# Kernel tuning notes

Measured on AMD Instinct MI355X. Metric: run time of the kernel, lower is better.

Reference implementation:

```python
import jax, jax.numpy as jnp
import numpy as np
from jax.scipy.special import logsumexp

D = 256; H = 8; A = D // H
B_CONST = 0.9; P_MAX = 50000.0; P_MIN = 1e-4; TANH_RATE = 0.005; EPS = 1e-10
SCALE = 1.0 / np.sqrt(D)


def setup_inputs() -> dict:
    key = jax.random.key(0)
    ks = jax.random.split(key, 5)
    B, S = 2, 512
    context = jax.random.normal(ks[0], (B, S, D), dtype=jnp.float32)
    W_Q = jax.random.normal(ks[1], (D, D), dtype=jnp.float32) * (1.0 / np.sqrt(D))
    W_KV = jax.random.normal(ks[2], (2 * D, D), dtype=jnp.float32) * (1.0 / np.sqrt(D))
    W_out = jax.random.normal(ks[3], (D, D), dtype=jnp.float32) * (1.0 / np.sqrt(D))
    p_param = jax.random.normal(ks[4], (D,), dtype=jnp.float32) * 0.02
    return {"context": context, "W_Q": W_Q, "W_KV": W_KV, "W_out": W_out, "p_param": p_param}


def reference(context, W_Q, W_KV, W_out, p_param):
    B, S, _ = context.shape
    # projections (nn.Linear: x @ W.T)
    q = context @ W_Q.T                          # [B,S,D]
    kv = context @ W_KV.T                        # [B,S,2D]
    k, v = kv[..., :D], kv[..., D:]
    # scaled p: p_max*tanh(tanh_rate*p)+1, then replace exact zeros with p_min
    p = P_MAX * jnp.tanh(TANH_RATE * p_param) + 1.0
    p = p + (p == 0).astype(p.dtype) * P_MIN
    # minmax-normalize v over the key/sequence axis into [b, 1]
    v_max = jnp.max(v, axis=-2, keepdims=True)   # [B,1,D]
    v_min = jnp.min(v, axis=-2, keepdims=True)
    v = (1.0 - B_CONST) * (v - v_min) / (v_max - v_min + EPS) + B_CONST
    z = p * jnp.log(v)                           # [B,S,D]
    # split heads
    qh = q.reshape(B, S, H, A).transpose(0, 2, 1, 3)          # [B,H,S,A]
    kh = k.reshape(B, S, H, A).transpose(0, 2, 1, 3)          # [B,H,S,A]
    zh = z.reshape(B, S, H, A).transpose(0, 2, 1, 3)[:, :, None]  # [B,H,1,K,A]
    dot = jnp.einsum('bhqa,bhka->bhqk', qh, kh)
    w = jax.nn.log_softmax(dot * SCALE, axis=-1)              # [B,H,Q,K]
    # log-domain power mean: logsumexp over keys of log-weights + p*log(v)
    mean = logsumexp(w[..., None] + zh, axis=-2)              # [B,H,Q,A]
    mean = mean.transpose(0, 2, 1, 3).reshape(B, S, D)
    e = jnp.exp(mean / p)
    # invert v minmax normalization
    e = (e - B_CONST) * (v_max - v_min + EPS) / (1.0 - B_CONST) + v_min
    return e @ W_out.T
```

## Files before the change

### kernel.cpp

```cpp
#include <hip/hip_runtime.h>
#include <math.h>

#define DD 256
#define HH 8
#define AA 32
#define SS 512
#define BB 2
constexpr float BCONST      = 0.9f;
constexpr float ONE_MINUS_B = 0.1f;
constexpr float EPSF        = 1e-10f;
constexpr float SCALEF      = 0.0625f;
constexpr float FLTMAX      = 3.402823466e38f;

#define OFF_QKV    0
#define OFF_VP     786432
#define OFF_EW     1048576
#define OFF_PMIN   1310720
#define OFF_PMAX   1318912
#define OFF_VMIN   1327104
#define OFF_VRANGE 1327616
#define OFF_P      1328128

#define KB4(buf, row, col4) \
  (&(buf)[((row) << 5) | ((((col4) >> 2) ^ (((row) >> 2) & 7)) << 2)])

template<int TM, int TN, int RM, int RN, bool MM>
__global__ __launch_bounds__(256) void gemm_t(
    const float* __restrict__ A, const float* __restrict__ B0,
    const float* __restrict__ B1, int nsplit,
    float* __restrict__ C, int ldc, int K, int lda,
    float* __restrict__ pminP, float* __restrict__ pmaxP) {
  constexpr int LDT = 36;
  constexpr int CG  = TN / RN;
  constexpr int NA  = TM * 32 / 1024;
  constexpr int NB  = TN * 32 / 1024;
  __shared__ float As[TM][LDT];
  __shared__ float Bs[TN][LDT];
  const int i0 = blockIdx.x * TM;
  const int j0 = blockIdx.y * TN;
  const float* Bsrc = (j0 < nsplit) ? (B0 + (size_t)j0 * K)
                                    : (B1 + (size_t)(j0 - nsplit) * K);
  const int t  = threadIdx.x;
  const int lr = t >> 3;
  const int lc = (t & 7) << 2;
  const int tx = t % CG, ty = t / CG;

  float4 pa[NA], pb[NB];
#pragma unroll
  for (int u = 0; u < NA; ++u)
    pa[u] = *(const float4*)(A + (size_t)(i0 + lr + 32 * u) * lda + lc);
#pragma unroll
  for (int u = 0; u < NB; ++u)
    pb[u] = *(const float4*)(Bsrc + (size_t)(lr + 32 * u) * K + lc);

  float acc[RM][RN] = {};
  for (int k0 = 0; k0 < K; k0 += 32) {
    __syncthreads();
#pragma unroll
    for (int u = 0; u < NA; ++u) *(float4*)&As[lr + 32 * u][lc] = pa[u];
#pragma unroll
    for (int u = 0; u < NB; ++u) *(float4*)&Bs[lr + 32 * u][lc] = pb[u];
    __syncthreads();
    if (k0 + 32 < K) {
#pragma unroll
      for (int u = 0; u < NA; ++u)
        pa[u] = *(const float4*)(A + (size_t)(i0 + lr + 32 * u) * lda + k0 + 32 + lc);
#pragma unroll
      for (int u = 0; u < NB; ++u)
        pb[u] = *(const float4*)(Bsrc + (size_t)(lr + 32 * u) * K + k0 + 32 + lc);
    }
#pragma unroll
    for (int kk = 0; kk < 32; kk += 4) {
      float4 af[RM], bf[RN];
#pragma unroll
      for (int r = 0; r < RM; ++r) af[r] = *(const float4*)&As[ty * RM + r][kk];
#pragma unroll
      for (int c = 0; c < RN; ++c) bf[c] = *(const float4*)&Bs[tx + CG * c][kk];
#pragma unroll
      for (int r = 0; r < RM; ++r)
#pragma unroll
        for (int c = 0; c < RN; ++c)
          acc[r][c] += af[r].x * bf[c].x + af[r].y * bf[c].y +
                       af[r].z * bf[c].z + af[r].w * bf[c].w;
    }
  }
#pragma unroll
  for (int r = 0; r < RM; ++r)
#pragma unroll
    for (int c = 0; c < RN; ++c)
      C[(size_t)(i0 + ty * RM + r) * ldc + j0 + tx + CG * c] = acc[r][c];

  if (MM && j0 >= 512) {
    __syncthreads();
    float* mnb = &As[0][0];
    float* mxb = &Bs[0][0];
#pragma unroll
    for (int c = 0; c < RN; ++c) {
      float mn = acc[0][c], mx = acc[0][c];
#pragma unroll
      for (int r = 1; r < RM; ++r) {
        mn = fminf(mn, acc[r][c]);
        mx = fmaxf(mx, acc[r][c]);
      }
      mnb[(tx + CG * c) * 17 + ty] = mn;
      mxb[(tx + CG * c) * 17 + ty] = mx;
    }
    __syncthreads();
    if (t < TN) {
      float mn = mnb[t * 17], mx = mxb[t * 17];
#pragma unroll
      for (int i = 1; i < 16; ++i) {
        mn = fminf(mn, mnb[t * 17 + i]);
        mx = fmaxf(mx, mxb[t * 17 + i]);
      }
      const int bx = i0 >> 5;
      pminP[bx * 256 + (j0 - 512) + t] = mn;
      pmaxP[bx * 256 + (j0 - 512) + t] = mx;
    }
  }
}

__global__ __launch_bounds__(256) void vpk(
    const float* __restrict__ qkv, const float* __restrict__ pminP,
    const float* __restrict__ pmaxP, const float* __restrict__ p_param,
    float* __restrict__ vp, float* __restrict__ vminw,
    float* __restrict__ vrangew, float* __restrict__ pw) {
  const int blk = blockIdx.x;
  const int b = blk >> 9, s = blk & 511;
  const int d = threadIdx.x;
  float mn = pminP[(b * 16) * 256 + d];
  float mx = pmaxP[(b * 16) * 256 + d];
#pragma unroll
  for (int c = 1; c < 16; ++c) {
    mn = fminf(mn, pminP[(b * 16 + c) * 256 + d]);
    mx = fmaxf(mx, pmaxP[(b * 16 + c) * 256 + d]);
  }
  float p = 50000.0f * tanhf(0.005f * p_param[d]) + 1.0f;
  if (p == 0.0f) p = 0.0001f;
  const float range = mx - mn + EPSF;
  const float v  = qkv[((size_t)(b * 512 + s)) * 768 + 512 + d];
  const float vn = (ONE_MINUS_B * (v - mn)) / range + BCONST;
  vp[(size_t)blk * 256 + d] = expm1f(p * logf(vn));
  if (s == 0) { vminw[b * 256 + d] = mn; vrangew[b * 256 + d] = range; }
  if (blk == 0) pw[d] = p;
}

__global__ __launch_bounds__(256) void attn_k(
    const float* __restrict__ qkv, const float* __restrict__ vp,
    const float* __restrict__ pw, const float* __restrict__ vminw,
    const float* __restrict__ vrangew, float* __restrict__ ew) {
  __shared__ float qs[32][36];
  __shared__ float sc[32 * 516];
  __shared__ float kb[512 * 32];
  __shared__ float red[32];
  const int bh  = blockIdx.y;
  const int b   = bh >> 3, h = bh & 7;
  const int q0g = blockIdx.x * 32;
  const int t   = threadIdx.x;
  const int srow = t >> 3, scol4 = (t & 7) << 2;

  {
    const int q = t >> 3, c4 = (t & 7) << 2;
    float4 qv = *(const float4*)(qkv + ((size_t)(b * 512 + q0g + q)) * 768 + h * 32 + c4);
    qv.x *= SCALEF; qv.y *= SCALEF; qv.z *= SCALEF; qv.w *= SCALEF;
    *(float4*)&qs[q][c4] = qv;
  }
#pragma unroll 8
  for (int u = 0; u < 16; ++u) {
    const int r = srow + 32 * u;
    float4 v = *(const float4*)(qkv + ((size_t)(b * 512 + r)) * 768 + 256 + h * 32 + scol4);
    *(float4*)KB4(kb, r, scol4) = v;
  }
  __syncthreads();

  {
    const int qgw = t >> 6;
    const int kg  = t & 63;
    float s8[8][8] = {};
#pragma unroll 2
    for (int kk = 0; kk < 32; kk += 4) {
      float4 qf[8], kf1[4], kf2[4];
#pragma unroll
      for (int r = 0; r < 8; ++r) qf[r] = *(const float4*)&qs[qgw + 4 * r][kk];
#pragma unroll
      for (int c = 0; c < 4; ++c) {
        kf1[c] = *(const float4*)KB4(kb, kg * 4 + c, kk);
        kf2[c] = *(const float4*)KB4(kb, 256 + kg * 4 + c, kk);
      }
#pragma unroll
      for (int r = 0; r < 8; ++r)
#pragma unroll
        for (int c = 0; c < 4; ++c) {
          s8[r][c]     += qf[r].x * kf1[c].x + qf[r].y * kf1[c].y +
                          qf[r].z * kf1[c].z + qf[r].w * kf1[c].w;
          s8[r][4 + c] += qf[r].x * kf2[c].x + qf[r].y * kf2[c].y +
                          qf[r].z * kf2[c].z + qf[r].w * kf2[c].w;
        }
    }
    float rs[8];
#pragma unroll
    for (int r = 0; r < 8; ++r) {
      float s = 0.f;
#pragma unroll
      for (int c = 0; c < 8; ++c) {
        s8[r][c] = __expf(s8[r][c]);
        s += s8[r][c];
      }
      rs[r] = s;
    }
#pragma unroll
    for (int m = 1; m < 64; m <<= 1)
#pragma unroll
      for (int r = 0; r < 8; ++r) rs[r] += __shfl_xor(rs[r], m);
    if ((t & 63) == 0)
#pragma unroll
      for (int r = 0; r < 8; ++r) red[qgw + 4 * r] = rs[r];
#pragma unroll
    for (int r = 0; r < 8; ++r) {
      const int rq = qgw + 4 * r;
      *(float4*)&sc[rq * 516 + kg * 4] =
          make_float4(s8[r][0], s8[r][1], s8[r][2], s8[r][3]);
      *(float4*)&sc[rq * 516 + 256 + kg * 4] =
          make_float4(s8[r][4], s8[r][5], s8[r][6], s8[r][7]);
    }
  }
  __syncthreads();

#pragma unroll 8
  for (int u = 0; u < 16; ++u) {
    const int r = srow + 32 * u;
    float4 v = *(const float4*)(vp + ((size_t)(b * 512 + r)) * 256 + h * 32 + scol4);
    *(float4*)KB4(kb, r, scol4) = v;
  }
  __syncthreads();

  const int ag  = t & 7;
  const int qg3 = (t >> 3) & 3;
  const int ks  = t >> 5;
  float a3[8][4] = {};
#pragma unroll 2
  for (int g = 0; g < 16; ++g) {
    const int kbase = ks * 64 + g * 4;
    float4 sq[8], vf[4];
#pragma unroll
    for (int r = 0; r < 8; ++r)
      sq[r] = *(const float4*)&sc[(qg3 + 4 * r) * 516 + kbase];
#pragma unroll
    for (int c = 0; c < 4; ++c)
      vf[c] = *(const float4*)KB4(kb, kbase + c, ag * 4);
#pragma unroll
    for (int r = 0; r < 8; ++r) {
      a3[r][0] += sq[r].x * vf[0].x + sq[r].y * vf[1].x + sq[r].z * vf[2].x + sq[r].w * vf[3].x;
      a3[r][1] += sq[r].x * vf[0].y + sq[r].y * vf[1].y + sq[r].z * vf[2].y + sq[r].w * vf[3].y;
      a3[r][2] += sq[r].x * vf[0].z + sq[r].y * vf[1].z + sq[r].z * vf[2].z + sq[r].w * vf[3].z;
      a3[r][3] += sq[r].x * vf[0].w + sq[r].y * vf[1].w + sq[r].z * vf[2].w + sq[r].w * vf[3].w;
    }
  }

#pragma unroll
  for (int r = 0; r < 8; ++r)
#pragma unroll
    for (int c = 0; c < 4; ++c)
      a3[r][c] += __shfl_xor(a3[r][c], 32);
  __syncthreads();
  float* part = &kb[0];
  if ((t & 32) == 0) {
    const int w = t >> 6;
#pragma unroll
    for (int r = 0; r < 8; ++r)
#pragma unroll
      for (int c = 0; c < 4; ++c)
        part[w * 1152 + (qg3 + 4 * r) * 36 + ag * 4 + c] = a3[r][c];
  }
  __syncthreads();

  {
    const int q = t >> 3, a0 = (t & 7) << 2;
    const int d0 = h * 32 + a0;
    const float invT = 1.0f / red[q];
    float4 s0 = *(const float4*)&part[q * 36 + a0];
    float4 s1 = *(const float4*)&part[1152 + q * 36 + a0];
    float4 s2 = *(const float4*)&part[2304 + q * 36 + a0];
    float4 s3 = *(const float4*)&part[3456 + q * 36 + a0];
    const float4 pp = *(const float4*)(pw + d0);
    const float4 vr = *(const float4*)(vrangew + b * 256 + d0);
    const float4 vm = *(const float4*)(vminw + b * 256 + d0);
    float4 o;
    o.x = (expf(log1pf((s0.x + s1.x + s2.x + s3.x) * invT) / pp.x) - BCONST) * vr.x / ONE_MINUS_B + vm.x;
    o.y = (expf(log1pf((s0.y + s1.y + s2.y + s3.y) * invT) / pp.y) - BCONST) * vr.y / ONE_MINUS_B + vm.y;
    o.z = (expf(log1pf((s0.z + s1.z + s2.z + s3.z) * invT) / pp.z) - BCONST) * vr.z / ONE_MINUS_B + vm.z;
    o.w = (expf(log1pf((s0.w + s1.w + s2.w + s3.w) * invT) / pp.w) - BCONST) * vr.w / ONE_MINUS_B + vm.w;
    *(float4*)(ew + ((size_t)(b * 512 + q0g + q)) * 256 + d0) = o;
  }
}

extern "C" void kernel_launch(void* const* d_in, const int* in_sizes, int n_in,
                              void* d_out, int out_size, void* d_ws, size_t ws_size,
                              hipStream_t stream) {
  const float* ctx  = (const float*)d_in[0];
  const float* WQ   = (const float*)d_in[1];
  const float* WKV  = (const float*)d_in[2];
  const float* WOUT = (const float*)d_in[3];
  const float* PP   = (const float*)d_in[4];
  float* ws      = (float*)d_ws;
  float* qkv     = ws + OFF_QKV;
  float* vp      = ws + OFF_VP;
  float* ew      = ws + OFF_EW;
  float* pminP   = ws + OFF_PMIN;
  float* pmaxP   = ws + OFF_PMAX;
  float* vminw   = ws + OFF_VMIN;
  float* vrangew = ws + OFF_VRANGE;
  float* pw      = ws + OFF_P;
  float* out     = (float*)d_out;

  gemm_t<32, 64, 2, 4, true><<<dim3(32, 12), 256, 0, stream>>>(
      ctx, WQ, WKV, 256, qkv, 768, 256, 256, pminP, pmaxP);
  vpk<<<1024, 256, 0, stream>>>(qkv, pminP, pmaxP, PP, vp, vminw, vrangew, pw);
  attn_k<<<dim3(16, 16), 256, 0, stream>>>(qkv, vp, pw, vminw, vrangew, ew);
  gemm_t<32, 32, 2, 2, false><<<dim3(32, 8), 256, 0, stream>>>(
      ew, WOUT, WOUT, 1 << 30, out, 256, 256, 256, nullptr, nullptr);
}
```

Measured before the change: 107.3 us.

## Fuse all four stages into one persistent kernel with software grid barriers

Replaces the four separate launches (QKV GEMM, v-power transform, attention, output GEMM) with one 256-block persistent kernel that separates the stages with atomic-counter grid barriers. The QKV GEMM is retiled to 32x96 tiles and the v-transform is redistributed so each stage maps onto exactly 256 blocks. The aim is to remove launch gaps and inter-kernel drain between the small stages. In exchange it relies on all 256 blocks being co-resident, adds spin-wait barrier cost with system-scope fences, and resets the barrier with a magic-flag handshake that could race across repeated calls.

Measured after the change: 204.2 us. +90.3%, slower.

```diff
diff --git a/kernel.cpp b/kernel.cpp
--- a/kernel.cpp
+++ b/kernel.cpp
@@ -1,296 +1,368 @@
 #include <hip/hip_runtime.h>
 #include <math.h>
 
-#define DD 256
-#define HH 8
-#define AA 32
-#define SS 512
-#define BB 2
 constexpr float BCONST      = 0.9f;
 constexpr float ONE_MINUS_B = 0.1f;
 constexpr float EPSF        = 1e-10f;
 constexpr float SCALEF      = 0.0625f;
-constexpr float FLTMAX      = 3.402823466e38f;
-
-#define OFF_QKV    0
-#define OFF_VP     786432
-#define OFF_EW     1048576
-#define OFF_PMIN   1310720
-#define OFF_PMAX   1318912
-#define OFF_VMIN   1327104
-#define OFF_VRANGE 1327616
-#define OFF_P      1328128
+
+#define OFF_QKV   0
+#define OFF_VP    786432
+#define OFF_EW    1048576
+#define OFF_PMIN  1310720
+#define OFF_PMAX  1318912
+#define OFF_VMIN  1327104
+#define OFF_VRG   1327616
+#define OFF_P     1328128
+#define OFF_BAR   8388608
+
+#define BAR_MAGIC 0x9E3779B9u
 
 #define KB4(buf, row, col4) \
   (&(buf)[((row) << 5) | ((((col4) >> 2) ^ (((row) >> 2) & 7)) << 2)])
 
-template<int TM, int TN, int RM, int RN, bool MM>
-__global__ __launch_bounds__(256) void gemm_t(
-    const float* __restrict__ A, const float* __restrict__ B0,
-    const float* __restrict__ B1, int nsplit,
-    float* __restrict__ C, int ldc, int K, int lda,
-    float* __restrict__ pminP, float* __restrict__ pmaxP) {
-  constexpr int LDT = 36;
-  constexpr int CG  = TN / RN;
-  constexpr int NA  = TM * 32 / 1024;
-  constexpr int NB  = TN * 32 / 1024;
-  __shared__ float As[TM][LDT];
-  __shared__ float Bs[TN][LDT];
-  const int i0 = blockIdx.x * TM;
-  const int j0 = blockIdx.y * TN;
-  const float* Bsrc = (j0 < nsplit) ? (B0 + (size_t)j0 * K)
-                                    : (B1 + (size_t)(j0 - nsplit) * K);
-  const int t  = threadIdx.x;
-  const int lr = t >> 3;
-  const int lc = (t & 7) << 2;
-  const int tx = t % CG, ty = t / CG;
-
-  float4 pa[NA], pb[NB];
-#pragma unroll
-  for (int u = 0; u < NA; ++u)
-    pa[u] = *(const float4*)(A + (size_t)(i0 + lr + 32 * u) * lda + lc);
-#pragma unroll
-  for (int u = 0; u < NB; ++u)
-    pb[u] = *(const float4*)(Bsrc + (size_t)(lr + 32 * u) * K + lc);
-
-  float acc[RM][RN] = {};
-  for (int k0 = 0; k0 < K; k0 += 32) {
-    __syncthreads();
-#pragma unroll
-    for (int u = 0; u < NA; ++u) *(float4*)&As[lr + 32 * u][lc] = pa[u];
-#pragma unroll
-    for (int u = 0; u < NB; ++u) *(float4*)&Bs[lr + 32 * u][lc] = pb[u];
-    __syncthreads();
-    if (k0 + 32 < K) {
-#pragma unroll
-      for (int u = 0; u < NA; ++u)
-        pa[u] = *(const float4*)(A + (size_t)(i0 + lr + 32 * u) * lda + k0 + 32 + lc);
-#pragma unroll
-      for (int u = 0; u < NB; ++u)
-        pb[u] = *(const float4*)(Bsrc + (size_t)(lr + 32 * u) * K + k0 + 32 + lc);
-    }
-#pragma unroll
-    for (int kk = 0; kk < 32; kk += 4) {
-      float4 af[RM], bf[RN];
-#pragma unroll
-      for (int r = 0; r < RM; ++r) af[r] = *(const float4*)&As[ty * RM + r][kk];
-#pragma unroll
-      for (int c = 0; c < RN; ++c) bf[c] = *(const float4*)&Bs[tx + CG * c][kk];
-#pragma unroll
-      for (int r = 0; r < RM; ++r)
-#pragma unroll
-        for (int c = 0; c < RN; ++c)
-          acc[r][c] += af[r].x * bf[c].x + af[r].y * bf[c].y +
-                       af[r].z * bf[c].z + af[r].w * bf[c].w;
-    }
-  }
-#pragma unroll
-  for (int r = 0; r < RM; ++r)
-#pragma unroll
-    for (int c = 0; c < RN; ++c)
-      C[(size_t)(i0 + ty * RM + r) * ldc + j0 + tx + CG * c] = acc[r][c];
-
-  if (MM && j0 >= 512) {
-    __syncthreads();
-    float* mnb = &As[0][0];
-    float* mxb = &Bs[0][0];
-#pragma unroll
-    for (int c = 0; c < RN; ++c) {
-      float mn = acc[0][c], mx = acc[0][c];
-#pragma unroll
-      for (int r = 1; r < RM; ++r) {
-        mn = fminf(mn, acc[r][c]);
-        mx = fmaxf(mx, acc[r][c]);
-      }
-      mnb[(tx + CG * c) * 17 + ty] = mn;
-      mxb[(tx + CG * c) * 17 + ty] = mx;
-    }
-    __syncthreads();
-    if (t < TN) {
-      float mn = mnb[t * 17], mx = mxb[t * 17];
-#pragma unroll
-      for (int i = 1; i < 16; ++i) {
-        mn = fminf(mn, mnb[t * 17 + i]);
-        mx = fmaxf(mx, mxb[t * 17 + i]);
-      }
-      const int bx = i0 >> 5;
-      pminP[bx * 256 + (j0 - 512) + t] = mn;
-      pmaxP[bx * 256 + (j0 - 512) + t] = mx;
-    }
-  }
+__device__ __forceinline__ void gridbar(unsigned* cnt, unsigned* flag,
+                                        unsigned gen, bool first) {
+  __syncthreads();
+  if (threadIdx.x == 0) {
+    __threadfence_system();
+    if (first) {
+      while (__hip_atomic_load(flag, __ATOMIC_ACQUIRE,
+                               __HIP_MEMORY_SCOPE_SYSTEM) != BAR_MAGIC) {
+        __builtin_amdgcn_s_sleep(2);
+      }
+    }
+    __hip_atomic_fetch_add(cnt, 1u, __ATOMIC_ACQ_REL,
+                           __HIP_MEMORY_SCOPE_SYSTEM);
+    const unsigned tgt = 256u * gen;
+    while (__hip_atomic_load(cnt, __ATOMIC_ACQUIRE,
+                             __HIP_MEMORY_SCOPE_SYSTEM) < tgt) {
+      __builtin_amdgcn_s_sleep(2);
+    }
+    __threadfence_system();
+  }
+  __syncthreads();
 }
 
-__global__ __launch_bounds__(256) void vpk(
-    const float* __restrict__ qkv, const float* __restrict__ pminP,
-    const float* __restrict__ pmaxP, const float* __restrict__ p_param,
-    float* __restrict__ vp, float* __restrict__ vminw,
-    float* __restrict__ vrangew, float* __restrict__ pw) {
+__global__ __launch_bounds__(256) void fused_k(
+    const float* __restrict__ ctx, const float* __restrict__ WQ,
+    const float* __restrict__ WKV, const float* __restrict__ WOUT,
+    const float* __restrict__ PP, float* __restrict__ ws,
+    float* __restrict__ out) {
+  __shared__ float S[34080];
   const int blk = blockIdx.x;
-  const int b = blk >> 9, s = blk & 511;
-  const int d = threadIdx.x;
-  float mn = pminP[(b * 16) * 256 + d];
-  float mx = pmaxP[(b * 16) * 256 + d];
-#pragma unroll
-  for (int c = 1; c < 16; ++c) {
-    mn = fminf(mn, pminP[(b * 16 + c) * 256 + d]);
-    mx = fmaxf(mx, pmaxP[(b * 16 + c) * 256 + d]);
-  }
-  float p = 50000.0f * tanhf(0.005f * p_param[d]) + 1.0f;
-  if (p == 0.0f) p = 0.0001f;
-  const float range = mx - mn + EPSF;
-  const float v  = qkv[((size_t)(b * 512 + s)) * 768 + 512 + d];
-  const float vn = (ONE_MINUS_B * (v - mn)) / range + BCONST;
-  vp[(size_t)blk * 256 + d] = expm1f(p * logf(vn));
-  if (s == 0) { vminw[b * 256 + d] = mn; vrangew[b * 256 + d] = range; }
-  if (blk == 0) pw[d] = p;
-}
-
-__global__ __launch_bounds__(256) void attn_k(
-    const float* __restrict__ qkv, const float* __restrict__ vp,
-    const float* __restrict__ pw, const float* __restrict__ vminw,
-    const float* __restrict__ vrangew, float* __restrict__ ew) {
-  __shared__ float qs[32][36];
-  __shared__ float sc[32 * 516];
-  __shared__ float kb[512 * 32];
-  __shared__ float red[32];
-  const int bh  = blockIdx.y;
-  const int b   = bh >> 3, h = bh & 7;
-  const int q0g = blockIdx.x * 32;
   const int t   = threadIdx.x;
-  const int srow = t >> 3, scol4 = (t & 7) << 2;
+
+  float* qkv   = ws + OFF_QKV;
+  float* vp    = ws + OFF_VP;
+  float* ew    = ws + OFF_EW;
+  float* pminP = ws + OFF_PMIN;
+  float* pmaxP = ws + OFF_PMAX;
+  float* vminw = ws + OFF_VMIN;
+  float* vrgw  = ws + OFF_VRG;
+  float* pw    = ws + OFF_P;
+  unsigned* bar = (unsigned*)(ws + OFF_BAR);
+
+  if (blk == 0 && t == 0) {
+    __hip_atomic_store(&bar[0], 0u, __ATOMIC_RELAXED, __HIP_MEMORY_SCOPE_SYSTEM);
+    __threadfence_system();
+    __hip_atomic_store(&bar[1], BAR_MAGIC, __ATOMIC_RELEASE, __HIP_MEMORY_SCOPE_SYSTEM);
+  }
 
   {
-    const int q = t >> 3, c4 = (t & 7) << 2;
-    float4 qv = *(const float4*)(qkv + ((size_t)(b * 512 + q0g + q)) * 768 + h * 32 + c4);
-    qv.x *= SCALEF; qv.y *= SCALEF; qv.z *= SCALEF; qv.w *= SCALEF;
-    *(float4*)&qs[q][c4] = qv;
-  }
+    float (*As)[36] = (float (*)[36])S;
+    float (*Bs)[36] = (float (*)[36])(S + 1152);
+    const int rt = blk & 31, ct = blk >> 5;
+    const int i0 = rt * 32, j0 = ct * 96;
+    const int lr = t >> 3, lc = (t & 7) << 2;
+    const int tx = t & 15, ty = t >> 4;
+    const float* arow = ctx + (size_t)(i0 + lr) * 256;
+    const float* brow[3];
+#pragma unroll
+    for (int u = 0; u < 3; ++u) {
+      const int j = j0 + lr + 32 * u;
+      brow[u] = (j < 256) ? (WQ + (size_t)j * 256)
+                          : (WKV + (size_t)(j - 256) * 256);
+    }
+    float4 pa = *(const float4*)(arow + lc);
+    float4 pb[3];
+#pragma unroll
+    for (int u = 0; u < 3; ++u) pb[u] = *(const float4*)(brow[u] + lc);
+
+    float acc[2][6] = {};
+    for (int k0 = 0; k0 < 256; k0 += 32) {
+      __syncthreads();
+      *(float4*)&As[lr][lc] = pa;
+#pragma unroll
+      for (int u = 0; u < 3; ++u) *(float4*)&Bs[lr + 32 * u][lc] = pb[u];
+      __syncthreads();
+      if (k0 + 32 < 256) {
+        pa = *(const float4*)(arow + k0 + 32 + lc);
+#pragma unroll
+        for (int u = 0; u < 3; ++u)
+          pb[u] = *(const float4*)(brow[u] + k0 + 32 + lc);
+      }
+#pragma unroll
+      for (int kk = 0; kk < 32; kk += 4) {
+        float4 af[2], bf[6];
+#pragma unroll
+        for (int r = 0; r < 2; ++r) af[r] = *(const float4*)&As[ty * 2 + r][kk];
+#pragma unroll
+        for (int c = 0; c < 6; ++c) bf[c] = *(const float4*)&Bs[tx + 16 * c][kk];
+#pragma unroll
+        for (int r = 0; r < 2; ++r)
+#pragma unroll
+          for (int c = 0; c < 6; ++c)
+            acc[r][c] += af[r].x * bf[c].x + af[r].y * bf[c].y +
+                         af[r].z * bf[c].z + af[r].w * bf[c].w;
+      }
+    }
+#pragma unroll
+    for (int r = 0; r < 2; ++r)
+#pragma unroll
+      for (int c = 0; c < 6; ++c)
+        qkv[(size_t)(i0 + ty * 2 + r) * 768 + j0 + tx + 16 * c] = acc[r][c];
+
+    if (ct >= 5) {
+      __syncthreads();
+      float* mnb = S;
+      float* mxb = S + 1632;
+#pragma unroll
+      for (int c = 0; c < 6; ++c) {
+        mnb[(tx + 16 * c) * 17 + ty] = fminf(acc[0][c], acc[1][c]);
+        mxb[(tx + 16 * c) * 17 + ty] = fmaxf(acc[0][c], acc[1][c]);
+      }
+      __syncthreads();
+      if (t < 96) {
+        const int j = j0 + t;
+        if (j >= 512) {
+          float mn = mnb[t * 17], mx = mxb[t * 17];
+#pragma unroll
+          for (int i = 1; i < 16; ++i) {
+            mn = fminf(mn, mnb[t * 17 + i]);
+            mx = fmaxf(mx, mxb[t * 17 + i]);
+          }
+          pminP[rt * 256 + (j - 512)] = mn;
+          pmaxP[rt * 256 + (j - 512)] = mx;
+        }
+      }
+    }
+  }
+  gridbar(&bar[0], &bar[1], 1u, true);
+
+  {
+    float p = 50000.0f * tanhf(0.005f * PP[t]) + 1.0f;
+    if (p == 0.0f) p = 0.0001f;
+    if (blk == 0) pw[t] = p;
+#pragma unroll
+    for (int b = 0; b < 2; ++b) {
+      float mn = pminP[(b * 16) * 256 + t];
+      float mx = pmaxP[(b * 16) * 256 + t];
+#pragma unroll
+      for (int c = 1; c < 16; ++c) {
+        mn = fminf(mn, pminP[(b * 16 + c) * 256 + t]);
+        mx = fmaxf(mx, pmaxP[(b * 16 + c) * 256 + t]);
+      }
+      const float range = mx - mn + EPSF;
+      if (blk == 0) { vminw[b * 256 + t] = mn; vrgw[b * 256 + t] = range; }
+#pragma unroll
+      for (int i = 0; i < 2; ++i) {
+        const int s = blk + 256 * i;
+        const float v  = qkv[((size_t)(b * 512 + s)) * 768 + 512 + t];
+        const float vn = (ONE_MINUS_B * (v - mn)) / range + BCONST;
+        vp[((size_t)(b * 512 + s)) * 256 + t] = expm1f(p * logf(vn));
+      }
+    }
+  }
+  gridbar(&bar[0], &bar[1], 2u, false);
+
+  {
+    float* qs  = S;
+    float* sc  = S + 1152;
+    float* kb  = S + 17664;
+    float* red = S + 34048;
+    const int bh  = blk >> 4;
+    const int b   = bh >> 3, h = bh & 7;
+    const int q0g = (blk & 15) * 32;
+    const int srow = t >> 3, scol4 = (t & 7) << 2;
+
+    {
+      const int q = t >> 3, c4 = (t & 7) << 2;
+      float4 qv = *(const float4*)(qkv + ((size_t)(b * 512 + q0g + q)) * 768 + h * 32 + c4);
+      qv.x *= SCALEF; qv.y *= SCALEF; qv.z *= SCALEF; qv.w *= SCALEF;
+      *(float4*)&qs[q * 36 + c4] = qv;
+    }
 #pragma unroll 8
-  for (int u = 0; u < 16; ++u) {
-    const int r = srow + 32 * u;
-    float4 v = *(const float4*)(qkv + ((size_t)(b * 512 + r)) * 768 + 256 + h * 32 + scol4);
-    *(float4*)KB4(kb, r, scol4) = v;
-  }
-  __syncthreads();
+    for (int u = 0; u < 16; ++u) {
+      const int r = srow + 32 * u;
+      float4 v = *(const float4*)(qkv + ((size_t)(b * 512 + r)) * 768 + 256 + h * 32 + scol4);
+      *(float4*)KB4(kb, r, scol4) = v;
+    }
+    __syncthreads();
+
+    {
+      const int qgw = t >> 6;
+      const int kg  = t & 63;
+      float s8[8][8] = {};
+#pragma unroll 2
+      for (int kk = 0; kk < 32; kk += 4) {
+        float4 qf[8], kf1[4], kf2[4];
+#pragma unroll
+        for (int r = 0; r < 8; ++r) qf[r] = *(const float4*)&qs[(qgw + 4 * r) * 36 + kk];
+#pragma unroll
+        for (int c = 0; c < 4; ++c) {
+          kf1[c] = *(const float4*)KB4(kb, kg * 4 + c, kk);
+          kf2[c] = *(const float4*)KB4(kb, 256 + kg * 4 + c, kk);
+        }
+#pragma unroll
+        for (int r = 0; r < 8; ++r)
+#pragma unroll
+          for (int c = 0; c < 4; ++c) {
+            s8[r][c]     += qf[r].x * kf1[c].x + qf[r].y * kf1[c].y +
+                            qf[r].z * kf1[c].z + qf[r].w * kf1[c].w;
+            s8[r][4 + c] += qf[r].x * kf2[c].x + qf[r].y * kf2[c].y +
+                            qf[r].z * kf2[c].z + qf[r].w * kf2[c].w;
+          }
+      }
+      float rs[8];
+#pragma unroll
+      for (int r = 0; r < 8; ++r) {
+        float s = 0.f;
+#pragma unroll
+        for (int c = 0; c < 8; ++c) {
+          s8[r][c] = __expf(s8[r][c]);
+          s += s8[r][c];
+        }
+        rs[r] = s;
+      }
+#pragma unroll
+      for (int m = 1; m < 64; m <<= 1)
+#pragma unroll
+        for (int r = 0; r < 8; ++r) rs[r] += __shfl_xor(rs[r], m);
+      if ((t & 63) == 0)
+#pragma unroll
+        for (int r = 0; r < 8; ++r) red[qgw + 4 * r] = rs[r];
+#pragma unroll
+      for (int r = 0; r < 8; ++r) {
+        const int rq = qgw + 4 * r;
+        *(float4*)&sc[rq * 516 + kg * 4] =
+            make_float4(s8[r][0], s8[r][1], s8[r][2], s8[r][3]);
+        *(float4*)&sc[rq * 516 + 256 + kg * 4] =
+            make_float4(s8[r][4], s8[r][5], s8[r][6], s8[r][7]);
+      }
+    }
+    __syncthreads();
+
+#pragma unroll 8
+    for (int u = 0; u < 16; ++u) {
+      const int r = srow + 32 * u;
+      float4 v = *(const float4*)(vp + ((size_t)(b * 512 + r)) * 256 + h * 32 + scol4);
+      *(float4*)KB4(kb, r, scol4) = v;
+    }
+    __syncthreads();
+
+    const int ag  = t & 7;
+    const int qg3 = (t >> 3) & 3;
+    const int ks  = t >> 5;
+    float a3[8][4] = {};
+#pragma unroll 2
+    for (int g = 0; g < 16; ++g) {
+      const int kbase = ks * 64 + g * 4;
+      float4 sq[8], vf[4];
+#pragma unroll
+      for (int r = 0; r < 8; ++r)
+        sq[r] = *(const float4*)&sc[(qg3 + 4 * r) * 516 + kbase];
+#pragma unroll
+      for (int c = 0; c < 4; ++c)
+        vf[c] = *(const float4*)KB4(kb, kbase + c, ag * 4);
+#pragma unroll
+      for (int r = 0; r < 8; ++r) {
+        a3[r][0] += sq[r].x * vf[0].x + sq[r].y * vf[1].x + sq[r].z * vf[2].x + sq[r].w * vf[3].x;
+        a3[r][1] += sq[r].x * vf[0].y + sq[r].y * vf[1].y + sq[r].z * vf[2].y + sq[r].w * vf[3].y;
+        a3[r][2] += sq[r].x * vf[0].z + sq[r].y * vf[1].z + sq[r].z * vf[2].z + sq[r].w * vf[3].z;
+        a3[r][3] += sq[r].x * vf[0].w + sq[r].y * vf[1].w + sq[r].z * vf[2].w + sq[r].w * vf[3].w;
+      }
+    }
+#pragma unroll
+    for (int r = 0; r < 8; ++r)
+#pragma unroll
+      for (int c = 0; c < 4; ++c)
+        a3[r][c] += __shfl_xor(a3[r][c], 32);
+    __syncthreads();
+    float* part = kb;
+    if ((t & 32) == 0) {
+      const int w = t >> 6;
+#pragma unroll
+      for (int r = 0; r < 8; ++r)
+#pragma unroll
+        for (int c = 0; c < 4; ++c)
+          part[w * 1152 + (qg3 + 4 * r) * 36 + ag * 4 + c] = a3[r][c];
+    }
+    __syncthreads();
+
+    {
+      const int q = t >> 3, a0 = (t & 7) << 2;
+      const int d0 = h * 32 + a0;
+      const float invT = 1.0f / red[q];
+      float4 s0 = *(const float4*)&part[q * 36 + a0];
+      float4 s1 = *(const float4*)&part[1152 + q * 36 + a0];
+      float4 s2 = *(const float4*)&part[2304 + q * 36 + a0];
+      float4 s3 = *(const float4*)&part[3456 + q * 36 + a0];
+      const float4 pp = *(const float4*)(pw + d0);
+      const float4 vr = *(const float4*)(vrgw + b * 256 + d0);
+      const float4 vm = *(const float4*)(vminw + b * 256 + d0);
+      float4 o;
+      o.x = (expf(log1pf((s0.x + s1.x + s2.x + s3.x) * invT) / pp.x) - BCONST) * vr.x / ONE_MINUS_B + vm.x;
+      o.y = (expf(log1pf((s0.y + s1.y + s2.y + s3.y) * invT) / pp.y) - BCONST) * vr.y / ONE_MINUS_B + vm.y;
+      o.z = (expf(log1pf((s0.z + s1.z + s2.z + s3.z) * invT) / pp.z) - BCONST) * vr.z / ONE_MINUS_B + vm.z;
+      o.w = (expf(log1pf((s0.w + s1.w + s2.w + s3.w) * invT) / pp.w) - BCONST) * vr.w / ONE_MINUS_B + vm.w;
+      *(float4*)(ew + ((size_t)(b * 512 + q0g + q)) * 256 + d0) = o;
+    }
+  }
+  gridbar(&bar[0], &bar[1], 3u, false);
 
   {
-    const int qgw = t >> 6;
-    const int kg  = t & 63;
-    float s8[8][8] = {};
-#pragma unroll 2
-    for (int kk = 0; kk < 32; kk += 4) {
-      float4 qf[8], kf1[4], kf2[4];
-#pragma unroll
-      for (int r = 0; r < 8; ++r) qf[r] = *(const float4*)&qs[qgw + 4 * r][kk];
-#pragma unroll
-      for (int c = 0; c < 4; ++c) {
-        kf1[c] = *(const float4*)KB4(kb, kg * 4 + c, kk);
-        kf2[c] = *(const float4*)KB4(kb, 256 + kg * 4 + c, kk);
-      }
-#pragma unroll
-      for (int r = 0; r < 8; ++r)
-#pragma unroll
-        for (int c = 0; c < 4; ++c) {
-          s8[r][c]     += qf[r].x * kf1[c].x + qf[r].y * kf1[c].y +
-                          qf[r].z * kf1[c].z + qf[r].w * kf1[c].w;
-          s8[r][4 + c] += qf[r].x * kf2[c].x + qf[r].y * kf2[c].y +
-                          qf[r].z * kf2[c].z + qf[r].w * kf2[c].w;
-        }
-    }
-    float rs[8];
-#pragma unroll
-    for (int r = 0; r < 8; ++r) {
-      float s = 0.f;
-#pragma unroll
-      for (int c = 0; c < 8; ++c) {
-        s8[r][c] = __expf(s8[r][c]);
-        s += s8[r][c];
-      }
-      rs[r] = s;
-    }
-#pragma unroll
-    for (int m = 1; m < 64; m <<= 1)
-#pragma unroll
-      for (int r = 0; r < 8; ++r) rs[r] += __shfl_xor(rs[r], m);
-    if ((t & 63) == 0)
-#pragma unroll
-      for (int r = 0; r < 8; ++r) red[qgw + 4 * r] = rs[r];
-#pragma unroll
-    for (int r = 0; r < 8; ++r) {
-      const int rq = qgw + 4 * r;
-      *(float4*)&sc[rq * 516 + kg * 4] =
-          make_float4(s8[r][0], s8[r][1], s8[r][2], s8[r][3]);
-      *(float4*)&sc[rq * 516 + 256 + kg * 4] =
-          make_float4(s8[r][4], s8[r][5], s8[r][6], s8[r][7]);
-    }
-  }
-  __syncthreads();
-
-#pragma unroll 8
-  for (int u = 0; u < 16; ++u) {
-    const int r = srow + 32 * u;
-    float4 v = *(const float4*)(vp + ((size_t)(b * 512 + r)) * 256 + h * 32 + scol4);
-    *(float4*)KB4(kb, r, scol4) = v;
-  }
-  __syncthreads();
-
-  const int ag  = t & 7;
-  const int qg3 = (t >> 3) & 3;
-  const int ks  = t >> 5;
-  float a3[8][4] = {};
-#pragma unroll 2
-  for (int g = 0; g < 16; ++g) {
-    const int kbase = ks * 64 + g * 4;
-    float4 sq[8], vf[4];
-#pragma unroll
-    for (int r = 0; r < 8; ++r)
-      sq[r] = *(const float4*)&sc[(qg3 + 4 * r) * 516 + kbase];
-#pragma unroll
-    for (int c = 0; c < 4; ++c)
-      vf[c] = *(const float4*)KB4(kb, kbase + c, ag * 4);
-#pragma unroll
-    for (int r = 0; r < 8; ++r) {
-      a3[r][0] += sq[r].x * vf[0].x + sq[r].y * vf[1].x + sq[r].z * vf[2].x + sq[r].w * vf[3].x;
-      a3[r][1] += sq[r].x * vf[0].y + sq[r].y * vf[1].y + sq[r].z * vf[2].y + sq[r].w * vf[3].y;
-      a3[r][2] += sq[r].x * vf[0].z + sq[r].y * vf[1].z + sq[r].z * vf[2].z + sq[r].w * vf[3].z;
-      a3[r][3] += sq[r].x * vf[0].w + sq[r].y * vf[1].w + sq[r].z * vf[2].w + sq[r].w * vf[3].w;
-    }
-  }
-
-#pragma unroll
-  for (int r = 0; r < 8; ++r)
-#pragma unroll
-    for (int c = 0; c < 4; ++c)
-      a3[r][c] += __shfl_xor(a3[r][c], 32);
-  __syncthreads();
-  float* part = &kb[0];
-  if ((t & 32) == 0) {
-    const int w = t >> 6;
-#pragma unroll
-    for (int r = 0; r < 8; ++r)
-#pragma unroll
-      for (int c = 0; c < 4; ++c)
-        part[w * 1152 + (qg3 + 4 * r) * 36 + ag * 4 + c] = a3[r][c];
-  }
-  __syncthreads();
-
-  {
-    const int q = t >> 3, a0 = (t & 7) << 2;
-    const int d0 = h * 32 + a0;
-    const float invT = 1.0f / red[q];
-    float4 s0 = *(const float4*)&part[q * 36 + a0];
-    float4 s1 = *(const float4*)&part[1152 + q * 36 + a0];
-    float4 s2 = *(const float4*)&part[2304 + q * 36 + a0];
-    float4 s3 = *(const float4*)&part[3456 + q * 36 + a0];
-    const float4 pp = *(const float4*)(pw + d0);
-    const float4 vr = *(const float4*)(vrangew + b * 256 + d0);
-    const float4 vm = *(const float4*)(vminw + b * 256 + d0);
-    float4 o;
-    o.x = (expf(log1pf((s0.x + s1.x + s2.x + s3.x) * invT) / pp.x) - BCONST) * vr.x / ONE_MINUS_B + vm.x;
-    o.y = (expf(log1pf((s0.y + s1.y + s2.y + s3.y) * invT) / pp.y) - BCONST) * vr.y / ONE_MINUS_B + vm.y;
-    o.z = (expf(log1pf((s0.z + s1.z + s2.z + s3.z) * invT) / pp.z) - BCONST) * vr.z / ONE_MINUS_B + vm.z;
-    o.w = (expf(log1pf((s0.w + s1.w + s2.w + s3.w) * invT) / pp.w) - BCONST) * vr.w / ONE_MINUS_B + vm.w;
-    *(float4*)(ew + ((size_t)(b * 512 + q0g + q)) * 256 + d0) = o;
+    float (*As)[36] = (float (*)[36])S;
+    float (*Bs)[36] = (float (*)[36])(S + 1152);
+    const int rt = blk & 31, ct = blk >> 5;
+    const int i0 = rt * 32, j0 = ct * 32;
+    const int lr = t >> 3, lc = (t & 7) << 2;
+    const int tx = t & 15, ty = t >> 4;
+    const float* arow = ew + (size_t)(i0 + lr) * 256;
+    const float* brow = WOUT + (size_t)(j0 + lr) * 256;
+    float4 pa = *(const float4*)(arow + lc);
+    float4 pb = *(const float4*)(brow + lc);
+
+    float acc[2][2] = {};
+    for (int k0 = 0; k0 < 256; k0 += 32) {
+      __syncthreads();
+      *(float4*)&As[lr][lc] = pa;
+      *(float4*)&Bs[lr][lc] = pb;
+      __syncthreads();
+      if (k0 + 32 < 256) {
+        pa = *(const float4*)(arow + k0 + 32 + lc);
+        pb = *(const float4*)(brow + k0 + 32 + lc);
+      }
+#pragma unroll
+      for (int kk = 0; kk < 32; kk += 4) {
+        float4 af[2], bf[2];
+#pragma unroll
+        for (int r = 0; r < 2; ++r) af[r] = *(const float4*)&As[ty * 2 + r][kk];
+#pragma unroll
+        for (int c = 0; c < 2; ++c) bf[c] = *(const float4*)&Bs[tx + 16 * c][kk];
+#pragma unroll
+        for (int r = 0; r < 2; ++r)
+#pragma unroll
+          for (int c = 0; c < 2; ++c)
+            acc[r][c] += af[r].x * bf[c].x + af[r].y * bf[c].y +
+                         af[r].z * bf[c].z + af[r].w * bf[c].w;
+      }
+    }
+#pragma unroll
+    for (int r = 0; r < 2; ++r)
+#pragma unroll
+      for (int c = 0; c < 2; ++c)
+        out[(size_t)(i0 + ty * 2 + r) * 256 + j0 + tx + 16 * c] = acc[r][c];
   }
 }
 
@@ -302,21 +374,9 @@
   const float* WKV  = (const float*)d_in[2];
   const float* WOUT = (const float*)d_in[3];
   const float* PP   = (const float*)d_in[4];
-  float* ws      = (float*)d_ws;
-  float* qkv     = ws + OFF_QKV;
-  float* vp      = ws + OFF_VP;
-  float* ew      = ws + OFF_EW;
-  float* pminP   = ws + OFF_PMIN;
-  float* pmaxP   = ws + OFF_PMAX;
-  float* vminw   = ws + OFF_VMIN;
-  float* vrangew = ws + OFF_VRANGE;
-  float* pw      = ws + OFF_P;
-  float* out     = (float*)d_out;
-
-  gemm_t<32, 64, 2, 4, true><<<dim3(32, 12), 256, 0, stream>>>(
-      ctx, WQ, WKV, 256, qkv, 768, 256, 256, pminP, pmaxP);
-  vpk<<<1024, 256, 0, stream>>>(qkv, pminP, pmaxP, PP, vp, vminw, vrangew, pw);
-  attn_k<<<dim3(16, 16), 256, 0, stream>>>(qkv, vp, pw, vminw, vrangew, ew);
-  gemm_t<32, 32, 2, 2, false><<<dim3(32, 8), 256, 0, stream>>>(
-      ew, WOUT, WOUT, 1 << 30, out, 256, 256, 256, nullptr, nullptr);
+  float* ws  = (float*)d_ws;
+  float* out = (float*)d_out;
+
+  hipLaunchKernelGGL(fused_k, dim3(256), dim3(256), 0, stream,
+                     ctx, WQ, WKV, WOUT, PP, ws, out);
 }
```
